# Optimization experiments

Measured on AMD Instinct MI355X. Metric: run time of the kernel, lower is better.

Reference implementation:

```python
import jax, jax.numpy as jnp
import numpy as np

N, E, F_IN, HID, L, G = 50000, 400000, 128, 64, 3, 512
HEADS = 4  # per-head dim C = HID = 64 (PyG TransformerConv: out_channels per head)


def setup_inputs() -> dict:
    key = jax.random.key(0)
    ks = jax.random.split(key, 16)
    x = jax.random.normal(ks[0], (N, F_IN), dtype=jnp.float32)
    edge_index = jax.random.randint(ks[1], (2, E), 0, N, dtype=jnp.int64)
    batch = jnp.sort(jax.random.randint(ks[2], (N,), 0, G, dtype=jnp.int64))
    s_in = 1.0 / np.sqrt(F_IN)
    s_h = 1.0 / np.sqrt(HID)
    lin0_w = jax.random.normal(ks[3], (F_IN, HID), dtype=jnp.float32) * s_in
    lin0_b = jnp.zeros((HID,), dtype=jnp.float32)
    # stacked per-layer params [L, ...]
    Wq = jax.random.normal(ks[4], (L, HID, HEADS * HID), dtype=jnp.float32) * s_h
    Wk = jax.random.normal(ks[5], (L, HID, HEADS * HID), dtype=jnp.float32) * s_h
    Wv = jax.random.normal(ks[6], (L, HID, HEADS * HID), dtype=jnp.float32) * s_h
    bq = jnp.zeros((L, HEADS * HID), dtype=jnp.float32)
    bk = jnp.zeros((L, HEADS * HID), dtype=jnp.float32)
    bv = jnp.zeros((L, HEADS * HID), dtype=jnp.float32)
    Ws = jax.random.normal(ks[7], (L, HID, HID), dtype=jnp.float32) * s_h
    bs = jnp.zeros((L, HID), dtype=jnp.float32)
    return {"x": x, "edge_index": edge_index, "batch": batch,
            "lin0_w": lin0_w, "lin0_b": lin0_b,
            "Wq": Wq, "bq": bq, "Wk": Wk, "bk": bk, "Wv": Wv, "bv": bv,
            "Ws": Ws, "bs": bs}


def _transformer_conv(h, src, dst, Wq, bq, Wk, bk, Wv, bv, Ws, bs):
    n = h.shape[0]
    C = Wq.shape[1] // HEADS
    q = (h @ Wq + bq).reshape(n, HEADS, C)
    k = (h @ Wk + bk).reshape(n, HEADS, C)
    v = (h @ Wv + bv).reshape(n, HEADS, C)
    # per-edge attention logits: query at dst, key at src  -> [E, H]
    scale = jnp.asarray(1.0 / np.sqrt(C), h.dtype)
    logits = jnp.einsum('ehc,ehc->eh', q[dst], k[src]) * scale
    # segment softmax over incoming edges of each destination node
    m = jax.ops.segment_max(logits, dst, num_segments=n)
    e = jnp.exp(logits - m[dst])
    denom = jax.ops.segment_sum(e, dst, num_segments=n)
    p = e / denom[dst]  # every edge's dst segment is nonempty
    agg = jax.ops.segment_sum(p[:, :, None] * v[src], dst, num_segments=n)  # [n,H,C]
    return agg.mean(axis=1) + h @ Ws + bs  # concat=False: head mean + root skip


def reference(x, edge_index, batch, lin0_w, lin0_b, Wq, bq, Wk, bk, Wv, bv, Ws, bs):
    src, dst = edge_index[0], edge_index[1]
    h = x @ lin0_w + lin0_b  # [N, HID]; dropout is identity in eval mode
    for l in range(L):
        h = jax.nn.relu(_transformer_conv(h, src, dst, Wq[l], bq[l], Wk[l], bk[l],
                                          Wv[l], bv[l], Ws[l], bs[l]))
    # global add pool over graphs
    return jax.ops.segment_sum(h, batch, num_segments=G)  # [G, HID]
```

## Files before the change

kernel.cpp:

```cpp
#include <hip/hip_runtime.h>
#include <math.h>

#define F_IN 128
#define HID 64
#define NLAYER 3
#define QSW 832
#define QS_ROW 320
#define KV_ROW 512

typedef unsigned short ushort_t;
typedef __bf16 bf16x8 __attribute__((ext_vector_type(8)));
typedef unsigned short u16x8 __attribute__((ext_vector_type(8)));
typedef float f32x4 __attribute__((ext_vector_type(4)));
typedef float f32x2 __attribute__((ext_vector_type(2)));

__device__ __forceinline__ ushort_t f2bf(float f) {
  unsigned u = __float_as_uint(f);
  u += 0x7fffu + ((u >> 16) & 1u);
  return (ushort_t)(u >> 16);
}
__device__ __forceinline__ float bf2f(ushort_t s) {
  return __uint_as_float(((unsigned)s) << 16);
}
__device__ __forceinline__ float blo(unsigned u) { return __uint_as_float(u << 16); }
__device__ __forceinline__ float bhi(unsigned u) { return __uint_as_float(u & 0xffff0000u); }

__device__ __forceinline__ void dec8(uint2 u, float* f) {
  f32x2 a0 = __builtin_amdgcn_cvt_pk_f32_fp8((int)u.x, false);
  f32x2 a1 = __builtin_amdgcn_cvt_pk_f32_fp8((int)u.x, true);
  f32x2 a2 = __builtin_amdgcn_cvt_pk_f32_fp8((int)u.y, false);
  f32x2 a3 = __builtin_amdgcn_cvt_pk_f32_fp8((int)u.y, true);
  f[0] = a0[0]; f[1] = a0[1]; f[2] = a1[0]; f[3] = a1[1];
  f[4] = a2[0]; f[5] = a2[1]; f[6] = a3[0]; f[7] = a3[1];
}

__global__ __launch_bounds__(256) void hist_k(const int* __restrict__ dst, int* __restrict__ cnt, int e) {
  int i = blockIdx.x * 256 + threadIdx.x;
  if (i < e) atomicAdd(&cnt[dst[i]], 1);
}
__global__ __launch_bounds__(1024) void scan_block_k(const int* __restrict__ cnt, int* __restrict__ excl,
                                                     int* __restrict__ bsum, int n) {
  __shared__ int tmp[1024];
  int t = threadIdx.x;
  int i = blockIdx.x * 1024 + t;
  int v = (i < n) ? cnt[i] : 0;
  tmp[t] = v;
  __syncthreads();
  for (int off = 1; off < 1024; off <<= 1) {
    int add = (t >= off) ? tmp[t - off] : 0;
    __syncthreads();
    tmp[t] += add;
    __syncthreads();
  }
  if (i < n) excl[i] = tmp[t] - v;
  if (t == 1023) bsum[blockIdx.x] = tmp[1023];
}
__global__ __launch_bounds__(64) void scan_bsum_k(int* __restrict__ bsum, int nb) {
  int l = threadIdx.x;
  int orig = (l < nb) ? bsum[l] : 0;
  int v = orig;
  for (int off = 1; off < 64; off <<= 1) {
    int u = __shfl_up(v, off);
    if (l >= off) v += u;
  }
  if (l < nb) bsum[l] = v - orig;
}
__global__ __launch_bounds__(256) void scatter_rowptr_k(const int* __restrict__ src, const int* __restrict__ dst,
                                                        const int* __restrict__ excl, const int* __restrict__ bsum,
                                                        int* __restrict__ cur, int* __restrict__ rowp,
                                                        int* __restrict__ srt, int n, int e) {
  int i = blockIdx.x * 256 + threadIdx.x;
  if (i < n) rowp[i] = excl[i] + bsum[i >> 10];
  if (i == 0) rowp[n] = e;
  if (i < e) {
    int d = dst[i];
    int pos = excl[d] + bsum[d >> 10] + atomicAdd(&cur[d], 1);
    srt[pos] = src[i];
  }
}

__global__ __launch_bounds__(64) void pack_weights(const float* __restrict__ Wq, const float* __restrict__ Wk,
                                                   const float* __restrict__ Wv, const float* __restrict__ Ws,
                                                   const float* __restrict__ w0,
                                                   const float* __restrict__ bq, const float* __restrict__ bk,
                                                   const float* __restrict__ bv, const float* __restrict__ bs,
                                                   ushort_t* __restrict__ wp_all, ushort_t* __restrict__ wp_lin0,
                                                   float* __restrict__ bp) {
  int b = blockIdx.x, lane = threadIdx.x;
  if (b < 312) {
    int l = b / 104, t = b % 104;
    int ntg = t >> 1, kt = t & 1;
    int col = ntg * 16 + (lane & 15);
    int kb = kt * 32 + (lane >> 4) * 8;
    const float* W;
    int c, stride;
    if (col < 256)      { W = Wq + (long long)l * 64 * 256; c = col;       stride = 256; }
    else if (col < 512) { W = Wk + (long long)l * 64 * 256; c = col - 256; stride = 256; }
    else if (col < 768) { W = Wv + (long long)l * 64 * 256; c = col - 512; stride = 256; }
    else                { W = Ws + (long long)l * 64 * 64;  c = col - 768; stride = 64; }
    ushort_t vals[8];
#pragma unroll
    for (int e = 0; e < 8; e++) vals[e] = f2bf(W[(long long)(kb + e) * stride + c]);
    ushort_t* p = wp_all + (long long)l * (104 * 512) + ((long long)t * 64 + lane) * 8;
    ushort4 lo{vals[0], vals[1], vals[2], vals[3]}, hi{vals[4], vals[5], vals[6], vals[7]};
    *(ushort4*)p = lo;
    *(ushort4*)(p + 4) = hi;
  } else if (b < 328) {
    int t = b - 312;
    int col = (t >> 2) * 16 + (lane & 15);
    int kb = (t & 3) * 32 + (lane >> 4) * 8;
    ushort_t vals[8];
#pragma unroll
    for (int e = 0; e < 8; e++) vals[e] = f2bf(w0[(long long)(kb + e) * 64 + col]);
    ushort_t* p = wp_lin0 + ((long long)t * 64 + lane) * 8;
    ushort4 lo{vals[0], vals[1], vals[2], vals[3]}, hi{vals[4], vals[5], vals[6], vals[7]};
    *(ushort4*)p = lo;
    *(ushort4*)(p + 4) = hi;
  } else {
    int l = b - 328;
    for (int c = lane; c < QSW; c += 64) {
      float v = (c < 256) ? bq[l * 256 + c]
              : (c < 512) ? bk[l * 256 + c - 256]
              : (c < 768) ? bv[l * 256 + c - 512]
              : bs[l * 64 + c - 768];
      bp[l * QSW + c] = v;
    }
  }
}

template <int K, int AF32, int MODE>
__global__ __launch_bounds__(256) void gemm_mfma(const void* __restrict__ Av, const ushort_t* __restrict__ Wp,
                                                 const float* __restrict__ bias, ushort_t* __restrict__ Cq,
                                                 unsigned char* __restrict__ Ckv, int n) {
  constexpr int KT = K / 32;
  int lane = threadIdx.x & 63;
  int wv = __builtin_amdgcn_readfirstlane((int)(threadIdx.x >> 6));
  int m0 = (blockIdx.x * 4 + wv) * 64;
  int n0 = blockIdx.y * 64;
  int lr = lane & 15, lq = lane >> 4;

  bf16x8 a[4][KT];
#pragma unroll
  for (int mr = 0; mr < 4; mr++) {
    int row = m0 + mr * 16 + lr;
    if (row >= n) row = n - 1;
    if constexpr (AF32) {
      const float* Af = (const float*)Av;
#pragma unroll
      for (int kt = 0; kt < KT; kt++) {
        const float* p = Af + (long long)row * K + kt * 32 + lq * 8;
        float4 f0 = *(const float4*)p;
        float4 f1 = *(const float4*)(p + 4);
        u16x8 u;
        u[0] = f2bf(f0.x); u[1] = f2bf(f0.y); u[2] = f2bf(f0.z); u[3] = f2bf(f0.w);
        u[4] = f2bf(f1.x); u[5] = f2bf(f1.y); u[6] = f2bf(f1.z); u[7] = f2bf(f1.w);
        a[mr][kt] = __builtin_bit_cast(bf16x8, u);
      }
    } else {
      const ushort_t* Ab = (const ushort_t*)Av;
#pragma unroll
      for (int kt = 0; kt < KT; kt++)
        a[mr][kt] = *(const bf16x8*)(Ab + (long long)row * K + kt * 32 + lq * 8);
    }
  }
  f32x4 acc[4][4];
#pragma unroll
  for (int nt = 0; nt < 4; nt++) {
    float4 b4 = *(const float4*)(bias + n0 + nt * 16 + lq * 4);
    f32x4 bi = {b4.x, b4.y, b4.z, b4.w};
#pragma unroll
    for (int mr = 0; mr < 4; mr++) acc[mr][nt] = bi;
  }
#pragma unroll
  for (int nt = 0; nt < 4; nt++) {
    int ntg = (n0 >> 4) + nt;
    bf16x8 bw[KT];
#pragma unroll
    for (int kt = 0; kt < KT; kt++)
      bw[kt] = *(const bf16x8*)(Wp + ((long long)(ntg * KT + kt) * 64 + lane) * 8);
#pragma unroll
    for (int kt = 0; kt < KT; kt++)
#pragma unroll
      for (int mr = 0; mr < 4; mr++)
        acc[mr][nt] = __builtin_amdgcn_mfma_f32_16x16x32_bf16(bw[kt], a[mr][kt], acc[mr][nt], 0, 0, 0);
  }
#pragma unroll
  for (int mr = 0; mr < 4; mr++) {
    int row = m0 + mr * 16 + lr;
    if (row >= n) continue;
    if constexpr (MODE == 0) {
#pragma unroll
      for (int nt = 0; nt < 4; nt++) {
        ushort4 o{f2bf(acc[mr][nt][0]), f2bf(acc[mr][nt][1]), f2bf(acc[mr][nt][2]), f2bf(acc[mr][nt][3])};
        *(ushort4*)(Cq + (long long)row * HID + n0 + nt * 16 + lq * 4) = o;
      }
    } else {
      if (blockIdx.y < 4) {
#pragma unroll
        for (int nt = 0; nt < 4; nt++) {
          ushort4 o{f2bf(acc[mr][nt][0]), f2bf(acc[mr][nt][1]), f2bf(acc[mr][nt][2]), f2bf(acc[mr][nt][3])};
          *(ushort4*)(Cq + (long long)row * QS_ROW + n0 + nt * 16 + lq * 4) = o;
        }
      } else if (blockIdx.y < 12) {
#pragma unroll
        for (int nt = 0; nt < 4; nt++) {
          int c = n0 - 256 + nt * 16 + lq * 4;
          int pk = __builtin_amdgcn_cvt_pk_fp8_f32(acc[mr][nt][0], acc[mr][nt][1], 0, false);
          pk = __builtin_amdgcn_cvt_pk_fp8_f32(acc[mr][nt][2], acc[mr][nt][3], pk, true);
          *(unsigned*)(Ckv + (long long)row * KV_ROW + c) = (unsigned)pk;
        }
      } else {
#pragma unroll
        for (int nt = 0; nt < 4; nt++) {
          int c = n0 - 768 + nt * 16 + lq * 4;
          ushort4 o{f2bf(acc[mr][nt][0]), f2bf(acc[mr][nt][1]), f2bf(acc[mr][nt][2]), f2bf(acc[mr][nt][3])};
          *(ushort4*)(Cq + (long long)row * QS_ROW + 256 + c) = o;
        }
      }
    }
  }
}

__global__ __launch_bounds__(256) void attn_k(const ushort_t* __restrict__ qs,
                                              const unsigned char* __restrict__ kv,
                                              const int* __restrict__ rowp, const int* __restrict__ srt,
                                              ushort_t* __restrict__ hn, int n) {
  int wvv = __builtin_amdgcn_readfirstlane((int)(threadIdx.x >> 6));
  int node = blockIdx.x * 4 + wvv;
  if (node >= n) return;
  int lane = threadIdx.x & 63;
  int half = lane >> 5;
  int sl = lane & 31;
  const uint4 qu = *(const uint4*)(qs + (long long)node * QS_ROW + sl * 8);
  float qf[8];
  qf[0] = blo(qu.x); qf[1] = bhi(qu.x); qf[2] = blo(qu.y); qf[3] = bhi(qu.y);
  qf[4] = blo(qu.z); qf[5] = bhi(qu.z); qf[6] = blo(qu.w); qf[7] = bhi(qu.w);
  int rs = rowp[node], re = rowp[node + 1];
  int last = re - 1;
  float m = -INFINITY, d = 0.f;
  float a[8];
#pragma unroll
  for (int j = 0; j < 8; j++) a[j] = 0.f;

  for (int i = rs; i < re; i += 8) {
    int b0 = i + half * 4;
    int j0 = min(b0, last), j1 = min(b0 + 1, last), j2 = min(b0 + 2, last), j3 = min(b0 + 3, last);
    int i0 = srt[j0], i1 = srt[j1], i2 = srt[j2], i3 = srt[j3];
    const unsigned char* p0 = kv + (long long)i0 * KV_ROW + sl * 8;
    const unsigned char* p1 = kv + (long long)i1 * KV_ROW + sl * 8;
    const unsigned char* p2 = kv + (long long)i2 * KV_ROW + sl * 8;
    const unsigned char* p3 = kv + (long long)i3 * KV_ROW + sl * 8;
    uint2 k0 = *(const uint2*)p0;
    uint2 k1 = *(const uint2*)p1;
    uint2 k2 = *(const uint2*)p2;
    uint2 k3 = *(const uint2*)p3;
    uint2 v0 = *(const uint2*)(p0 + 256);
    uint2 v1 = *(const uint2*)(p1 + 256);
    uint2 v2 = *(const uint2*)(p2 + 256);
    uint2 v3 = *(const uint2*)(p3 + 256);
    float kf0[8], kf1[8], kf2[8], kf3[8];
    dec8(k0, kf0); dec8(k1, kf1); dec8(k2, kf2); dec8(k3, kf3);
    float t0 = 0.f, t1 = 0.f, t2 = 0.f, t3 = 0.f;
#pragma unroll
    for (int j = 0; j < 8; j++) {
      t0 = fmaf(qf[j], kf0[j], t0);
      t1 = fmaf(qf[j], kf1[j], t1);
      t2 = fmaf(qf[j], kf2[j], t2);
      t3 = fmaf(qf[j], kf3[j], t3);
    }
    t0 += __shfl_xor(t0, 1); t1 += __shfl_xor(t1, 1); t2 += __shfl_xor(t2, 1); t3 += __shfl_xor(t3, 1);
    t0 += __shfl_xor(t0, 2); t1 += __shfl_xor(t1, 2); t2 += __shfl_xor(t2, 2); t3 += __shfl_xor(t3, 2);
    t0 += __shfl_xor(t0, 4); t1 += __shfl_xor(t1, 4); t2 += __shfl_xor(t2, 4); t3 += __shfl_xor(t3, 4);
    t0 *= 0.125f; t1 *= 0.125f; t2 *= 0.125f; t3 *= 0.125f;
    if (b0 > last) t0 = -INFINITY;
    if (b0 + 1 > last) t1 = -INFINITY;
    if (b0 + 2 > last) t2 = -INFINITY;
    if (b0 + 3 > last) t3 = -INFINITY;
    float lm = fmaxf(fmaxf(t0, t1), fmaxf(t2, t3));
    lm = fmaxf(lm, __shfl_xor(lm, 32));
    if (__any(lm > m + 8.f)) {
      float mn = fmaxf(m, lm);
      float co = __expf(m - mn);
      d *= co;
#pragma unroll
      for (int j = 0; j < 8; j++) a[j] *= co;
      m = mn;
    }
    float p0e = __expf(t0 - m), p1e = __expf(t1 - m), p2e = __expf(t2 - m), p3e = __expf(t3 - m);
    d += (p0e + p1e) + (p2e + p3e);
    float vf0[8], vf1[8], vf2[8], vf3[8];
    dec8(v0, vf0); dec8(v1, vf1); dec8(v2, vf2); dec8(v3, vf3);
#pragma unroll
    for (int j = 0; j < 8; j++)
      a[j] += fmaf(p0e, vf0[j], p1e * vf1[j]) + fmaf(p2e, vf2[j], p3e * vf3[j]);
  }
  d += __shfl_xor(d, 32);
#pragma unroll
  for (int j = 0; j < 8; j++) a[j] += __shfl_xor(a[j], 32);
  float inv = (d > 0.f) ? 1.f / d : 0.f;
  float r[8];
#pragma unroll
  for (int j = 0; j < 8; j++) {
    r[j] = a[j] * inv;
    r[j] += __shfl_xor(r[j], 8);
    r[j] += __shfl_xor(r[j], 16);
  }
  if (lane < 8) {
    const u16x8 s8 = *(const u16x8*)(qs + (long long)node * QS_ROW + 256 + lane * 8);
    u16x8 o;
#pragma unroll
    for (int j = 0; j < 8; j++)
      o[j] = f2bf(fmaxf(r[j] * 0.25f + bf2f(s8[j]), 0.f));
    *(u16x8*)(hn + (long long)node * HID + lane * 8) = o;
  }
}

#define POOL_NPB 128
__global__ __launch_bounds__(64) void pool_k(const ushort_t* __restrict__ h, const int* __restrict__ batch,
                                             float* __restrict__ out, int n) {
  int c = threadIdx.x;
  int n0 = blockIdx.x * POOL_NPB;
  int n1 = n0 + POOL_NPB;
  if (n1 > n) n1 = n;
  if (n0 >= n) return;
  float acc = 0.f;
  int g = batch[n0];
  for (int node = n0; node < n1; node++) {
    int gb = batch[node];
    if (gb != g) {
      atomicAdd(&out[g * 64 + c], acc);
      acc = 0.f;
      g = gb;
    }
    acc += bf2f(h[(long long)node * 64 + c]);
  }
  atomicAdd(&out[g * 64 + c], acc);
}

extern "C" void kernel_launch(void* const* d_in, const int* in_sizes, int n_in,
                              void* d_out, int out_size, void* d_ws, size_t ws_size,
                              hipStream_t stream) {
  const float* x  = (const float*)d_in[0];
  const int* ei   = (const int*)d_in[1];
  const int* batch = (const int*)d_in[2];
  const float* w0 = (const float*)d_in[3];
  const float* b0 = (const float*)d_in[4];
  const float* Wq = (const float*)d_in[5];
  const float* bq = (const float*)d_in[6];
  const float* Wk = (const float*)d_in[7];
  const float* bk = (const float*)d_in[8];
  const float* Wv = (const float*)d_in[9];
  const float* bv = (const float*)d_in[10];
  const float* Ws = (const float*)d_in[11];
  const float* bs = (const float*)d_in[12];
  int N = in_sizes[0] / F_IN;
  int E = in_sizes[1] / 2;
  const int* esrc = ei;
  const int* edst = ei + E;

  float* bp = (float*)d_ws;
  unsigned char* kvb = (unsigned char*)(bp + 3 * QSW);
  ushort_t* h0 = (ushort_t*)(kvb + (size_t)N * KV_ROW);
  ushort_t* h1 = h0 + (long long)N * HID;
  ushort_t* qs = h1 + (long long)N * HID;
  ushort_t* wp_all  = qs + (long long)N * QS_ROW;
  ushort_t* wp_lin0 = wp_all + 3 * 104 * 512;
  int* cnt  = (int*)(wp_lin0 + 16 * 512);
  int* cur  = cnt + N;
  int* excl = cur + N;
  int* rowp = excl + N;
  int* bsum = rowp + N + 1;
  int* srt  = bsum + 64;

  int nbE = (E + 255) / 256;
  int sbBlocks = (N + 1023) / 1024;

  hipMemsetAsync(cnt, 0, (size_t)2 * N * sizeof(int), stream);
  hist_k<<<nbE, 256, 0, stream>>>(edst, cnt, E);
  scan_block_k<<<sbBlocks, 1024, 0, stream>>>(cnt, excl, bsum, N);
  scan_bsum_k<<<1, 64, 0, stream>>>(bsum, sbBlocks);
  scatter_rowptr_k<<<nbE, 256, 0, stream>>>(esrc, edst, excl, bsum, cur, rowp, srt, N, E);

  pack_weights<<<331, 64, 0, stream>>>(Wq, Wk, Wv, Ws, w0, bq, bk, bv, bs, wp_all, wp_lin0, bp);

  int mBlocks = (N + 255) / 256;

  gemm_mfma<128, 1, 0><<<dim3(mBlocks, 1), 256, 0, stream>>>(x, wp_lin0, b0, h0, nullptr, N);

  ushort_t* hc = h0;
  ushort_t* hx = h1;
  for (int l = 0; l < NLAYER; l++) {
    gemm_mfma<64, 0, 1><<<dim3(mBlocks, 13), 256, 0, stream>>>(hc, wp_all + (long long)l * 104 * 512,
                                                               bp + l * QSW, qs, kvb, N);
    attn_k<<<(N + 3) / 4, 256, 0, stream>>>(qs, kvb, rowp, srt, hx, N);
    ushort_t* t = hc; hc = hx; hx = t;
  }

  hipMemsetAsync(d_out, 0, (size_t)out_size * sizeof(float), stream);
  pool_k<<<(N + POOL_NPB - 1) / POOL_NPB, 64, 0, stream>>>(hc, batch, (float*)d_out, N);
}
```

Before: 333.0 us.

## Fold lin0 into layer-0 QKVS weights and restructure projection GEMM tiling

Precomputes W0·[Wq|Wk|Wv|Ws] and the matching folded bias so that layer 0's projection reads x directly (K=128). This removes the separate lin0 GEMM and the h0 round trip. The projection GEMM also changes shape: each wave now handles 32 rows and loops over 26 column tiles, with 2 y-blocks instead of 13, so A is loaded once per tile and reused across many columns. The trade-off is less parallelism and a non-unrolled column loop, plus a slightly different bf16 rounding path for the folded weights.

```diff
diff --git a/kernel.cpp b/kernel.cpp
--- a/kernel.cpp
+++ b/kernel.cpp
@@ -79,69 +79,91 @@
   }
 }
 
-__global__ __launch_bounds__(64) void pack_weights(const float* __restrict__ Wq, const float* __restrict__ Wk,
-                                                   const float* __restrict__ Wv, const float* __restrict__ Ws,
-                                                   const float* __restrict__ w0,
-                                                   const float* __restrict__ bq, const float* __restrict__ bk,
-                                                   const float* __restrict__ bv, const float* __restrict__ bs,
-                                                   ushort_t* __restrict__ wp_all, ushort_t* __restrict__ wp_lin0,
-                                                   float* __restrict__ bp) {
+__global__ __launch_bounds__(64) void pack2_k(const float* __restrict__ Wq, const float* __restrict__ Wk,
+                                              const float* __restrict__ Wv, const float* __restrict__ Ws,
+                                              const float* __restrict__ w0, const float* __restrict__ b0,
+                                              const float* __restrict__ bq, const float* __restrict__ bk,
+                                              const float* __restrict__ bv, const float* __restrict__ bs,
+                                              ushort_t* __restrict__ wp0, ushort_t* __restrict__ wp12,
+                                              float* __restrict__ bp) {
   int b = blockIdx.x, lane = threadIdx.x;
-  if (b < 312) {
-    int l = b / 104, t = b % 104;
+  if (b < 208) {
+    int ntg = b >> 2, kt = b & 3;
+    int col = ntg * 16 + (lane & 15);
+    int kb = kt * 32 + (lane >> 4) * 8;
+    const float* W; int c, stride;
+    if (col < 256)      { W = Wq; c = col;       stride = 256; }
+    else if (col < 512) { W = Wk; c = col - 256; stride = 256; }
+    else if (col < 768) { W = Wv; c = col - 512; stride = 256; }
+    else                { W = Ws; c = col - 768; stride = 64; }
+    float vals[8] = {0.f, 0.f, 0.f, 0.f, 0.f, 0.f, 0.f, 0.f};
+    for (int j = 0; j < 64; j++) {
+      float wj = W[(long long)j * stride + c];
+#pragma unroll
+      for (int e = 0; e < 8; e++) vals[e] = fmaf(w0[(kb + e) * 64 + j], wj, vals[e]);
+    }
+    ushort_t* p = wp0 + ((long long)b * 64 + lane) * 8;
+    ushort4 lo{f2bf(vals[0]), f2bf(vals[1]), f2bf(vals[2]), f2bf(vals[3])};
+    ushort4 hi{f2bf(vals[4]), f2bf(vals[5]), f2bf(vals[6]), f2bf(vals[7])};
+    *(ushort4*)p = lo;
+    *(ushort4*)(p + 4) = hi;
+  } else if (b < 416) {
+    int idx = b - 208;
+    int l = 1 + idx / 104, t = idx % 104;
     int ntg = t >> 1, kt = t & 1;
     int col = ntg * 16 + (lane & 15);
     int kb = kt * 32 + (lane >> 4) * 8;
-    const float* W;
-    int c, stride;
+    const float* W; int c, stride;
     if (col < 256)      { W = Wq + (long long)l * 64 * 256; c = col;       stride = 256; }
     else if (col < 512) { W = Wk + (long long)l * 64 * 256; c = col - 256; stride = 256; }
     else if (col < 768) { W = Wv + (long long)l * 64 * 256; c = col - 512; stride = 256; }
     else                { W = Ws + (long long)l * 64 * 64;  c = col - 768; stride = 64; }
-    ushort_t vals[8];
-#pragma unroll
-    for (int e = 0; e < 8; e++) vals[e] = f2bf(W[(long long)(kb + e) * stride + c]);
-    ushort_t* p = wp_all + (long long)l * (104 * 512) + ((long long)t * 64 + lane) * 8;
-    ushort4 lo{vals[0], vals[1], vals[2], vals[3]}, hi{vals[4], vals[5], vals[6], vals[7]};
-    *(ushort4*)p = lo;
-    *(ushort4*)(p + 4) = hi;
-  } else if (b < 328) {
-    int t = b - 312;
-    int col = (t >> 2) * 16 + (lane & 15);
-    int kb = (t & 3) * 32 + (lane >> 4) * 8;
-    ushort_t vals[8];
-#pragma unroll
-    for (int e = 0; e < 8; e++) vals[e] = f2bf(w0[(long long)(kb + e) * 64 + col]);
-    ushort_t* p = wp_lin0 + ((long long)t * 64 + lane) * 8;
-    ushort4 lo{vals[0], vals[1], vals[2], vals[3]}, hi{vals[4], vals[5], vals[6], vals[7]};
+    float vals[8];
+#pragma unroll
+    for (int e = 0; e < 8; e++) vals[e] = W[(long long)(kb + e) * stride + c];
+    ushort_t* p = wp12 + (long long)(l - 1) * (104 * 512) + ((long long)t * 64 + lane) * 8;
+    ushort4 lo{f2bf(vals[0]), f2bf(vals[1]), f2bf(vals[2]), f2bf(vals[3])};
+    ushort4 hi{f2bf(vals[4]), f2bf(vals[5]), f2bf(vals[6]), f2bf(vals[7])};
     *(ushort4*)p = lo;
     *(ushort4*)(p + 4) = hi;
   } else {
-    int l = b - 328;
-    for (int c = lane; c < QSW; c += 64) {
-      float v = (c < 256) ? bq[l * 256 + c]
-              : (c < 512) ? bk[l * 256 + c - 256]
-              : (c < 768) ? bv[l * 256 + c - 512]
-              : bs[l * 64 + c - 768];
-      bp[l * QSW + c] = v;
-    }
-  }
-}
-
-template <int K, int AF32, int MODE>
-__global__ __launch_bounds__(256) void gemm_mfma(const void* __restrict__ Av, const ushort_t* __restrict__ Wp,
-                                                 const float* __restrict__ bias, ushort_t* __restrict__ Cq,
-                                                 unsigned char* __restrict__ Ckv, int n) {
+    int l = b - 416;
+    if (l == 0) {
+      for (int c = lane; c < QSW; c += 64) {
+        const float* W; const float* borig; int cc, stride;
+        if (c < 256)      { W = Wq; borig = bq; cc = c;       stride = 256; }
+        else if (c < 512) { W = Wk; borig = bk; cc = c - 256; stride = 256; }
+        else if (c < 768) { W = Wv; borig = bv; cc = c - 512; stride = 256; }
+        else              { W = Ws; borig = bs; cc = c - 768; stride = 64; }
+        float acc = borig[cc];
+        for (int j = 0; j < 64; j++) acc = fmaf(b0[j], W[(long long)j * stride + cc], acc);
+        bp[c] = acc;
+      }
+    } else {
+      for (int c = lane; c < QSW; c += 64) {
+        float v = (c < 256) ? bq[l * 256 + c]
+                : (c < 512) ? bk[l * 256 + c - 256]
+                : (c < 768) ? bv[l * 256 + c - 512]
+                : bs[l * 64 + c - 768];
+        bp[l * QSW + c] = v;
+      }
+    }
+  }
+}
+
+template <int K, int AF32>
+__global__ __launch_bounds__(256) void gemm_fused(const void* __restrict__ Av, const ushort_t* __restrict__ Wp,
+                                                  const float* __restrict__ bias, ushort_t* __restrict__ Cq,
+                                                  unsigned char* __restrict__ Ckv, int n) {
   constexpr int KT = K / 32;
   int lane = threadIdx.x & 63;
   int wv = __builtin_amdgcn_readfirstlane((int)(threadIdx.x >> 6));
-  int m0 = (blockIdx.x * 4 + wv) * 64;
-  int n0 = blockIdx.y * 64;
+  int m0 = (blockIdx.x * 4 + wv) * 32;
   int lr = lane & 15, lq = lane >> 4;
 
-  bf16x8 a[4][KT];
-#pragma unroll
-  for (int mr = 0; mr < 4; mr++) {
+  bf16x8 a[2][KT];
+#pragma unroll
+  for (int mr = 0; mr < 2; mr++) {
     int row = m0 + mr * 16 + lr;
     if (row >= n) row = n - 1;
     if constexpr (AF32) {
@@ -163,59 +185,54 @@
         a[mr][kt] = *(const bf16x8*)(Ab + (long long)row * K + kt * 32 + lq * 8);
     }
   }
-  f32x4 acc[4][4];
-#pragma unroll
-  for (int nt = 0; nt < 4; nt++) {
-    float4 b4 = *(const float4*)(bias + n0 + nt * 16 + lq * 4);
-    f32x4 bi = {b4.x, b4.y, b4.z, b4.w};
-#pragma unroll
-    for (int mr = 0; mr < 4; mr++) acc[mr][nt] = bi;
-  }
-#pragma unroll
-  for (int nt = 0; nt < 4; nt++) {
-    int ntg = (n0 >> 4) + nt;
+  int row0 = m0 + lr, row1 = m0 + 16 + lr;
+  bool ok0 = row0 < n, ok1 = row1 < n;
+  int ntg0 = blockIdx.y * 26;
+#pragma unroll 1
+  for (int ntg = ntg0; ntg < ntg0 + 26; ntg++) {
+    float4 b4 = *(const float4*)(bias + ntg * 16 + lq * 4);
+    f32x4 acc0 = {b4.x, b4.y, b4.z, b4.w};
+    f32x4 acc1 = acc0;
     bf16x8 bw[KT];
 #pragma unroll
     for (int kt = 0; kt < KT; kt++)
       bw[kt] = *(const bf16x8*)(Wp + ((long long)(ntg * KT + kt) * 64 + lane) * 8);
 #pragma unroll
-    for (int kt = 0; kt < KT; kt++)
-#pragma unroll
-      for (int mr = 0; mr < 4; mr++)
-        acc[mr][nt] = __builtin_amdgcn_mfma_f32_16x16x32_bf16(bw[kt], a[mr][kt], acc[mr][nt], 0, 0, 0);
-  }
-#pragma unroll
-  for (int mr = 0; mr < 4; mr++) {
-    int row = m0 + mr * 16 + lr;
-    if (row >= n) continue;
-    if constexpr (MODE == 0) {
-#pragma unroll
-      for (int nt = 0; nt < 4; nt++) {
-        ushort4 o{f2bf(acc[mr][nt][0]), f2bf(acc[mr][nt][1]), f2bf(acc[mr][nt][2]), f2bf(acc[mr][nt][3])};
-        *(ushort4*)(Cq + (long long)row * HID + n0 + nt * 16 + lq * 4) = o;
+    for (int kt = 0; kt < KT; kt++) {
+      acc0 = __builtin_amdgcn_mfma_f32_16x16x32_bf16(bw[kt], a[0][kt], acc0, 0, 0, 0);
+      acc1 = __builtin_amdgcn_mfma_f32_16x16x32_bf16(bw[kt], a[1][kt], acc1, 0, 0, 0);
+    }
+    if (ntg < 16) {
+      int c = ntg * 16 + lq * 4;
+      if (ok0) {
+        ushort4 o{f2bf(acc0[0]), f2bf(acc0[1]), f2bf(acc0[2]), f2bf(acc0[3])};
+        *(ushort4*)(Cq + (long long)row0 * QS_ROW + c) = o;
+      }
+      if (ok1) {
+        ushort4 o{f2bf(acc1[0]), f2bf(acc1[1]), f2bf(acc1[2]), f2bf(acc1[3])};
+        *(ushort4*)(Cq + (long long)row1 * QS_ROW + c) = o;
+      }
+    } else if (ntg < 48) {
+      int c = ntg * 16 - 256 + lq * 4;
+      if (ok0) {
+        int pk = __builtin_amdgcn_cvt_pk_fp8_f32(acc0[0], acc0[1], 0, false);
+        pk = __builtin_amdgcn_cvt_pk_fp8_f32(acc0[2], acc0[3], pk, true);
+        *(unsigned*)(Ckv + (long long)row0 * KV_ROW + c) = (unsigned)pk;
+      }
+      if (ok1) {
+        int pk = __builtin_amdgcn_cvt_pk_fp8_f32(acc1[0], acc1[1], 0, false);
+        pk = __builtin_amdgcn_cvt_pk_fp8_f32(acc1[2], acc1[3], pk, true);
+        *(unsigned*)(Ckv + (long long)row1 * KV_ROW + c) = (unsigned)pk;
       }
     } else {
-      if (blockIdx.y < 4) {
-#pragma unroll
-        for (int nt = 0; nt < 4; nt++) {
-          ushort4 o{f2bf(acc[mr][nt][0]), f2bf(acc[mr][nt][1]), f2bf(acc[mr][nt][2]), f2bf(acc[mr][nt][3])};
-          *(ushort4*)(Cq + (long long)row * QS_ROW + n0 + nt * 16 + lq * 4) = o;
-        }
-      } else if (blockIdx.y < 12) {
-#pragma unroll
-        for (int nt = 0; nt < 4; nt++) {
-          int c = n0 - 256 + nt * 16 + lq * 4;
-          int pk = __builtin_amdgcn_cvt_pk_fp8_f32(acc[mr][nt][0], acc[mr][nt][1], 0, false);
-          pk = __builtin_amdgcn_cvt_pk_fp8_f32(acc[mr][nt][2], acc[mr][nt][3], pk, true);
-          *(unsigned*)(Ckv + (long long)row * KV_ROW + c) = (unsigned)pk;
-        }
-      } else {
-#pragma unroll
-        for (int nt = 0; nt < 4; nt++) {
-          int c = n0 - 768 + nt * 16 + lq * 4;
-          ushort4 o{f2bf(acc[mr][nt][0]), f2bf(acc[mr][nt][1]), f2bf(acc[mr][nt][2]), f2bf(acc[mr][nt][3])};
-          *(ushort4*)(Cq + (long long)row * QS_ROW + 256 + c) = o;
-        }
+      int c = ntg * 16 - 768 + lq * 4;
+      if (ok0) {
+        ushort4 o{f2bf(acc0[0]), f2bf(acc0[1]), f2bf(acc0[2]), f2bf(acc0[3])};
+        *(ushort4*)(Cq + (long long)row0 * QS_ROW + 256 + c) = o;
+      }
+      if (ok1) {
+        ushort4 o{f2bf(acc1[0]), f2bf(acc1[1]), f2bf(acc1[2]), f2bf(acc1[3])};
+        *(ushort4*)(Cq + (long long)row1 * QS_ROW + 256 + c) = o;
       }
     }
   }
@@ -360,12 +377,12 @@
 
   float* bp = (float*)d_ws;
   unsigned char* kvb = (unsigned char*)(bp + 3 * QSW);
-  ushort_t* h0 = (ushort_t*)(kvb + (size_t)N * KV_ROW);
-  ushort_t* h1 = h0 + (long long)N * HID;
-  ushort_t* qs = h1 + (long long)N * HID;
-  ushort_t* wp_all  = qs + (long long)N * QS_ROW;
-  ushort_t* wp_lin0 = wp_all + 3 * 104 * 512;
-  int* cnt  = (int*)(wp_lin0 + 16 * 512);
+  ushort_t* ha = (ushort_t*)(kvb + (size_t)N * KV_ROW);
+  ushort_t* hb = ha + (long long)N * HID;
+  ushort_t* qs = hb + (long long)N * HID;
+  ushort_t* wp0  = qs + (long long)N * QS_ROW;
+  ushort_t* wp12 = wp0 + 208 * 512;
+  int* cnt  = (int*)(wp12 + 2 * 104 * 512);
   int* cur  = cnt + N;
   int* excl = cur + N;
   int* rowp = excl + N;
@@ -381,21 +398,17 @@
   scan_bsum_k<<<1, 64, 0, stream>>>(bsum, sbBlocks);
   scatter_rowptr_k<<<nbE, 256, 0, stream>>>(esrc, edst, excl, bsum, cur, rowp, srt, N, E);
 
-  pack_weights<<<331, 64, 0, stream>>>(Wq, Wk, Wv, Ws, w0, bq, bk, bv, bs, wp_all, wp_lin0, bp);
-
-  int mBlocks = (N + 255) / 256;
-
-  gemm_mfma<128, 1, 0><<<dim3(mBlocks, 1), 256, 0, stream>>>(x, wp_lin0, b0, h0, nullptr, N);
-
-  ushort_t* hc = h0;
-  ushort_t* hx = h1;
-  for (int l = 0; l < NLAYER; l++) {
-    gemm_mfma<64, 0, 1><<<dim3(mBlocks, 13), 256, 0, stream>>>(hc, wp_all + (long long)l * 104 * 512,
-                                                               bp + l * QSW, qs, kvb, N);
-    attn_k<<<(N + 3) / 4, 256, 0, stream>>>(qs, kvb, rowp, srt, hx, N);
-    ushort_t* t = hc; hc = hx; hx = t;
-  }
+  pack2_k<<<419, 64, 0, stream>>>(Wq, Wk, Wv, Ws, w0, b0, bq, bk, bv, bs, wp0, wp12, bp);
+
+  int gBlocks = (N + 127) / 128;
+
+  gemm_fused<128, 1><<<dim3(gBlocks, 2), 256, 0, stream>>>(x, wp0, bp, qs, kvb, N);
+  attn_k<<<(N + 3) / 4, 256, 0, stream>>>(qs, kvb, rowp, srt, ha, N);
+  gemm_fused<64, 0><<<dim3(gBlocks, 2), 256, 0, stream>>>(ha, wp12, bp + QSW, qs, kvb, N);
+  attn_k<<<(N + 3) / 4, 256, 0, stream>>>(qs, kvb, rowp, srt, hb, N);
+  gemm_fused<64, 0><<<dim3(gBlocks, 2), 256, 0, stream>>>(hb, wp12 + 104 * 512, bp + 2 * QSW, qs, kvb, N);
+  attn_k<<<(N + 3) / 4, 256, 0, stream>>>(qs, kvb, rowp, srt, ha, N);
 
   hipMemsetAsync(d_out, 0, (size_t)out_size * sizeof(float), stream);
-  pool_k<<<(N + POOL_NPB - 1) / POOL_NPB, 64, 0, stream>>>(hc, batch, (float*)d_out, N);
-}
+  pool_k<<<(N + POOL_NPB - 1) / POOL_NPB, 64, 0, stream>>>(ha, batch, (float*)d_out, N);
+}
```

After: 380.7 us. 1.14x slower.
